# Performance work log

Hardware: AMD Instinct MI355X
Metric: run time of the kernel (lower is better)

Reference implementation:

```python
import jax, jax.numpy as jnp
import numpy as np


def _mlp(x, W1, b1, W2, b2):
    # Linear -> exact GELU (torch nn.GELU default) -> Linear
    h = jax.nn.gelu(x @ W1 + b1, approximate=False)
    return h @ W2 + b2


def setup_inputs() -> dict:
    B, L, H, NB, D, HID = 4, 4096, 16, 64, 1024, 128
    NS = H * NB
    key = jax.random.key(0)
    ks = jax.random.split(key, 6)
    theta_path = jax.random.normal(ks[0], (B, L, H, NB), dtype=jnp.float32)
    content_emb = jax.random.normal(ks[1], (B, L, D), dtype=jnp.float32)
    log_Pi = jnp.zeros((H, NB), dtype=jnp.float32)
    s1 = 1.0 / np.sqrt(D)
    s2 = 1.0 / np.sqrt(HID)
    # log_R_head: Linear(D,128) -> GELU -> Linear(128,NS), last weight scaled by 0.01, bias 0
    Wr1 = jax.random.uniform(ks[2], (D, HID), jnp.float32, -s1, s1)
    br1 = jnp.zeros((HID,), jnp.float32)
    Wr2 = jax.random.uniform(ks[3], (HID, NS), jnp.float32, -s2, s2) * 0.01
    br2 = jnp.zeros((NS,), jnp.float32)
    # measure_head: Linear(D,128) -> GELU -> Linear(128,NS)
    Wm1 = jax.random.uniform(ks[4], (D, HID), jnp.float32, -s1, s1)
    bm1 = jnp.zeros((HID,), jnp.float32)
    Wm2 = jax.random.uniform(ks[5], (HID, NS), jnp.float32, -s2, s2)
    bm2 = jnp.zeros((NS,), jnp.float32)
    return {
        "theta_path": theta_path, "content_emb": content_emb, "log_Pi": log_Pi,
        "Wr1": Wr1, "br1": br1, "Wr2": Wr2, "br2": br2,
        "Wm1": Wm1, "bm1": bm1, "Wm2": Wm2, "bm2": bm2,
    }


def reference(theta_path, content_emb, log_Pi, Wr1, br1, Wr2, br2, Wm1, bm1, Wm2, bm2):
    B, L, H, NB = theta_path.shape
    # per-token measurement noise R_t
    log_R = jnp.clip(_mlp(content_emb, Wr1, br1, Wr2, br2).reshape(B, L, H, NB), -5.0, 5.0)
    R = jnp.exp(log_R)
    # measurement z in (-pi, pi)
    z = jnp.pi * jnp.tanh(_mlp(content_emb, Wm1, bm1, Wm2, bm2).reshape(B, L, H, NB))
    diff = z - theta_path
    nu = jnp.arctan2(jnp.sin(diff), jnp.cos(diff))  # wrapped innovation
    Pi = jnp.exp(log_Pi)            # (H, NB) constant covariance
    Pi_b = Pi[None, None]           # (1,1,H,NB)
    K = Pi_b / jnp.maximum(Pi_b + R, 1e-8)  # Kalman gain
    alpha = 1.0 - K
    u = K * nu
    # scalar affine parallel scan: d[t] = alpha[t]*d[t-1] + u[t], d[-1]=0
    def combine(c1, c2):
        a1, v1 = c1
        a2, v2 = c2
        return a1 * a2, a2 * v1 + v2
    _, d = jax.lax.associative_scan(combine, (alpha, u), axis=1)
    theta_hat = theta_path + d
    return theta_hat, Pi, K, R
```

## Files before the change

kernel.cpp:

```cpp
#include <hip/hip_runtime.h>
#include <math.h>

static constexpr size_t OUT_THETA = 0;
static constexpr size_t OUT_PI    = 16777216;
static constexpr size_t OUT_K     = 16778240;
static constexpr size_t OUT_R     = 33555456;

#define PI_F     3.14159265358979323846f
#define INV2PI_F 0.15915494309189535f
#define PI2_HI   6.28318548202514648f
#define PI2_LO  -1.7484556e-7f
#define SPLIT_S  2048.0f
#define SPLIT_IS (1.0f / 2048.0f)

typedef _Float16 half8 __attribute__((ext_vector_type(8)));
typedef float    f32x4 __attribute__((ext_vector_type(4)));

__device__ __forceinline__ float gelu_f(float x) {
    return 0.5f * x * (1.0f + erff(x * 0.70710678118654752f));
}

__global__ __launch_bounds__(256) void k_prep(
    const float* __restrict__ Wr1, const float* __restrict__ Wm1,
    const float* __restrict__ Wr2, const float* __restrict__ Wm2,
    _Float16* __restrict__ W1rT, _Float16* __restrict__ W1mTh, _Float16* __restrict__ W1mTl,
    _Float16* __restrict__ W2rT, _Float16* __restrict__ W2mTh, _Float16* __restrict__ W2mTl)
{
    const int i = blockIdx.x * 256 + threadIdx.x;
    {
        const int k = i >> 7, c = i & 127;
        const int o = c * 1024 + k;
        W1rT[o] = (_Float16)Wr1[i];
        float w = Wm1[i];
        _Float16 h = (_Float16)w;
        W1mTh[o] = h;
        W1mTl[o] = (_Float16)((w - (float)h) * SPLIT_S);
    }
    {
        const int k = i >> 10, c = i & 1023;
        const int o = c * 128 + k;
        W2rT[o] = (_Float16)Wr2[i];
        float w = Wm2[i];
        _Float16 h = (_Float16)w;
        W2mTh[o] = h;
        W2mTl[o] = (_Float16)((w - (float)h) * SPLIT_S);
    }
}

__global__ __launch_bounds__(256, 3) void k_mm1(
    const float* __restrict__ X,
    const _Float16* __restrict__ WrT,
    const _Float16* __restrict__ WmTh, const _Float16* __restrict__ WmTl,
    const float* __restrict__ br1, const float* __restrict__ bm1,
    _Float16* __restrict__ OHr, _Float16* __restrict__ OHmh, _Float16* __restrict__ OHml)
{
    __shared__ _Float16 sm[15360];
    _Float16* WR = sm;
    _Float16* WH = sm + 5120;
    _Float16* WL = sm + 10240;

    const int m0   = blockIdx.x * 64;
    const int tid  = threadIdx.x;
    const int lane = tid & 63;
    const int quad = lane >> 4, l15 = lane & 15;
    const int rt   = tid >> 6;

    f32x4 accR[8] = {};
    f32x4 accA[8] = {};
    f32x4 accB[8] = {};

    const float* xp = X + (size_t)(m0 + rt * 16 + l15) * 1024 + quad * 8;
    float4 xa = *(const float4*)(xp);
    float4 xb = *(const float4*)(xp + 4);

    half8 wr[2], wh[2], wl[2];
#pragma unroll
    for (int it = 0; it < 2; ++it) {
        const int u = tid + it * 256;
        const int col = u >> 2, ws = u & 3;
        const size_t go = (size_t)col * 1024 + ws * 8;
        wr[it] = *(const half8*)(WrT  + go);
        wh[it] = *(const half8*)(WmTh + go);
        wl[it] = *(const half8*)(WmTl + go);
    }

    for (int k0 = 0; k0 < 1024; k0 += 32) {
        __syncthreads();
#pragma unroll
        for (int it = 0; it < 2; ++it) {
            const int u = tid + it * 256;
            const int col = u >> 2, ws = u & 3;
            *(half8*)&WR[col * 40 + ws * 8] = wr[it];
            *(half8*)&WH[col * 40 + ws * 8] = wh[it];
            *(half8*)&WL[col * 40 + ws * 8] = wl[it];
        }
        __syncthreads();
        half8 ah, al;
#pragma unroll
        for (int c = 0; c < 8; ++c) {
            float v = (c < 4) ? ((const float*)&xa)[c] : ((const float*)&xb)[c - 4];
            _Float16 h = (_Float16)v;
            ah[c] = h;
            al[c] = (_Float16)((v - (float)h) * SPLIT_S);
        }
        if (k0 + 32 < 1024) {
            xa = *(const float4*)(xp + k0 + 32);
            xb = *(const float4*)(xp + k0 + 36);
#pragma unroll
            for (int it = 0; it < 2; ++it) {
                const int u = tid + it * 256;
                const int col = u >> 2, ws = u & 3;
                const size_t go = (size_t)col * 1024 + k0 + 32 + ws * 8;
                wr[it] = *(const half8*)(WrT  + go);
                wh[it] = *(const half8*)(WmTh + go);
                wl[it] = *(const half8*)(WmTl + go);
            }
        }
#pragma unroll
        for (int ct = 0; ct < 8; ++ct) {
            half8 bhr = *(const half8*)&WR[(ct * 16 + l15) * 40 + quad * 8];
            accR[ct] = __builtin_amdgcn_mfma_f32_16x16x32_f16(ah, bhr, accR[ct], 0, 0, 0);
            half8 bhm = *(const half8*)&WH[(ct * 16 + l15) * 40 + quad * 8];
            accA[ct] = __builtin_amdgcn_mfma_f32_16x16x32_f16(ah, bhm, accA[ct], 0, 0, 0);
            half8 blm = *(const half8*)&WL[(ct * 16 + l15) * 40 + quad * 8];
            accB[ct] = __builtin_amdgcn_mfma_f32_16x16x32_f16(ah, blm, accB[ct], 0, 0, 0);
            accB[ct] = __builtin_amdgcn_mfma_f32_16x16x32_f16(al, bhm, accB[ct], 0, 0, 0);
        }
    }
#pragma unroll
    for (int ct = 0; ct < 8; ++ct) {
        const int col = ct * 16 + l15;
        const float bR = br1[col];
        const float bM = bm1[col];
#pragma unroll
        for (int reg = 0; reg < 4; ++reg) {
            const int token = m0 + rt * 16 + quad * 4 + reg;
            const size_t o = (size_t)token * 128 + col;
            float gr = gelu_f(accR[ct][reg] + bR);
            OHr[o] = (_Float16)gr;
            float gm = gelu_f(accA[ct][reg] + accB[ct][reg] * SPLIT_IS + bM);
            _Float16 h = (_Float16)gm;
            OHmh[o] = h;
            OHml[o] = (_Float16)((gm - (float)h) * SPLIT_S);
        }
    }
}

__global__ __launch_bounds__(256, 4) void k_mm2(
    const _Float16* __restrict__ Hr, const _Float16* __restrict__ Hmh, const _Float16* __restrict__ Hml,
    const _Float16* __restrict__ W2rT, const _Float16* __restrict__ W2mTh, const _Float16* __restrict__ W2mTl,
    const float* __restrict__ br2, const float* __restrict__ bm2,
    const float* __restrict__ log_Pi, const float* __restrict__ theta,
    float* __restrict__ out, float* __restrict__ Aws, float* __restrict__ Uws)
{
    __shared__ _Float16 sm[15360];
    _Float16* AHr = sm;
    _Float16* AHm = sm + 2560;
    _Float16* ALm = sm + 5120;
    _Float16* BHr = sm + 7680;
    _Float16* BHm = sm + 10240;
    _Float16* BLm = sm + 12800;

    const int tt = blockIdx.x;
    const int jt = blockIdx.y;
    const int m0 = tt * 64, n0 = jt * 64;
    const int tid  = threadIdx.x;
    const int lane = tid & 63;
    const int quad = lane >> 4, l15 = lane & 15;
    const int ct   = tid >> 6;
    const int row  = tid >> 2, seg = tid & 3;

    f32x4 accr[4] = {};
    f32x4 accA[4] = {};
    f32x4 accB[4] = {};

    const size_t aobase = (size_t)(m0 + row) * 128 + seg * 8;
    const size_t bobase = (size_t)(n0 + row) * 128 + seg * 8;
    half8 la = *(const half8*)(Hr    + aobase);
    half8 lb = *(const half8*)(Hmh   + aobase);
    half8 lc = *(const half8*)(Hml   + aobase);
    half8 ld = *(const half8*)(W2rT  + bobase);
    half8 le = *(const half8*)(W2mTh + bobase);
    half8 lf = *(const half8*)(W2mTl + bobase);

    for (int k0 = 0; k0 < 128; k0 += 32) {
        __syncthreads();
        const int so = row * 40 + seg * 8;
        *(half8*)&AHr[so] = la;
        *(half8*)&AHm[so] = lb;
        *(half8*)&ALm[so] = lc;
        *(half8*)&BHr[so] = ld;
        *(half8*)&BHm[so] = le;
        *(half8*)&BLm[so] = lf;
        __syncthreads();
        if (k0 + 32 < 128) {
            la = *(const half8*)(Hr    + aobase + k0 + 32);
            lb = *(const half8*)(Hmh   + aobase + k0 + 32);
            lc = *(const half8*)(Hml   + aobase + k0 + 32);
            ld = *(const half8*)(W2rT  + bobase + k0 + 32);
            le = *(const half8*)(W2mTh + bobase + k0 + 32);
            lf = *(const half8*)(W2mTl + bobase + k0 + 32);
        }
        const int bidx = (ct * 16 + l15) * 40 + quad * 8;
        half8 br_ = *(const half8*)&BHr[bidx];
        half8 bm_ = *(const half8*)&BHm[bidx];
        half8 bl_ = *(const half8*)&BLm[bidx];
#pragma unroll
        for (int rt = 0; rt < 4; ++rt) {
            const int aidx = (rt * 16 + l15) * 40 + quad * 8;
            half8 a_r = *(const half8*)&AHr[aidx];
            half8 a_h = *(const half8*)&AHm[aidx];
            half8 a_l = *(const half8*)&ALm[aidx];
            accr[rt] = __builtin_amdgcn_mfma_f32_16x16x32_f16(a_r, br_, accr[rt], 0, 0, 0);
            accA[rt] = __builtin_amdgcn_mfma_f32_16x16x32_f16(a_h, bm_, accA[rt], 0, 0, 0);
            accB[rt] = __builtin_amdgcn_mfma_f32_16x16x32_f16(a_h, bl_, accB[rt], 0, 0, 0);
            accB[rt] = __builtin_amdgcn_mfma_f32_16x16x32_f16(a_l, bm_, accB[rt], 0, 0, 0);
        }
    }

    const int col = n0 + ct * 16 + l15;
    const float Pi_  = expf(log_Pi[col]);
    const float b2rv = br2[col];
    const float b2mv = bm2[col];
    float segA[4], segU[4];
#pragma unroll
    for (int rt = 0; rt < 4; ++rt) {
        float A = 1.0f, U = 0.0f;
#pragma unroll
        for (int reg = 0; reg < 4; ++reg) {
            const int token = m0 + rt * 16 + quad * 4 + reg;
            const size_t idx = (size_t)token * 1024 + col;
            float lr = fminf(fmaxf(accr[rt][reg] + b2rv, -5.0f), 5.0f);
            float R  = expf(lr);
            float Kg = __fdividef(Pi_, fmaxf(Pi_ + R, 1e-8f));
            float zp = accA[rt][reg] + accB[rt][reg] * SPLIT_IS + b2mv;
            float z  = PI_F * tanhf(zp);
            float d  = z - theta[idx];
            float n  = rintf(d * INV2PI_F);
            float nu = fmaf(-n, PI2_HI, d);
            nu       = fmaf(-n, PI2_LO, nu);
            float u  = Kg * nu;
            float al = 1.0f - Kg;
            U = fmaf(al, U, u);
            A *= al;
            out[OUT_K + idx]     = Kg;
            out[OUT_R + idx]     = R;
            out[OUT_THETA + idx] = u;
        }
        segA[rt] = A; segU[rt] = U;
    }
    __syncthreads();
    float* cA = (float*)sm;
    float* cU = cA + 1088;
    const int colLocal = ct * 16 + l15;
#pragma unroll
    for (int rt = 0; rt < 4; ++rt) {
        cA[colLocal * 17 + rt * 4 + quad] = segA[rt];
        cU[colLocal * 17 + rt * 4 + quad] = segU[rt];
    }
    __syncthreads();
    if (tid < 64) {
        float A = 1.0f, U = 0.0f;
#pragma unroll
        for (int s = 0; s < 16; ++s) {
            float a = cA[tid * 17 + s];
            float u = cU[tid * 17 + s];
            U = fmaf(a, U, u);
            A *= a;
        }
        Aws[(size_t)tt * 1024 + n0 + tid] = A;
        Uws[(size_t)tt * 1024 + n0 + tid] = U;
    }
}

__global__ __launch_bounds__(256) void k_carry(
    const float* __restrict__ Aws, const float* __restrict__ Uws, float* __restrict__ Cws,
    const float* __restrict__ log_Pi, float* __restrict__ out)
{
    const int b  = blockIdx.x;
    const int j4 = threadIdx.x;
    if (b == 0) {
        float4 lp = *(const float4*)(log_Pi + j4 * 4);
        float4 p;
        p.x = expf(lp.x); p.y = expf(lp.y); p.z = expf(lp.z); p.w = expf(lp.w);
        *(float4*)(out + OUT_PI + j4 * 4) = p;
    }
    float4 carry = {0.0f, 0.0f, 0.0f, 0.0f};
#pragma unroll 8
    for (int c = 0; c < 64; ++c) {
        const size_t off = (size_t)(b * 64 + c) * 1024 + j4 * 4;
        float4 a = *(const float4*)(Aws + off);
        float4 u = *(const float4*)(Uws + off);
        *(float4*)(Cws + off) = carry;
        carry.x = fmaf(a.x, carry.x, u.x);
        carry.y = fmaf(a.y, carry.y, u.y);
        carry.z = fmaf(a.z, carry.z, u.z);
        carry.w = fmaf(a.w, carry.w, u.w);
    }
}

__global__ __launch_bounds__(256) void k_apply(
    const float* __restrict__ theta, const float* __restrict__ Cws, float* __restrict__ out)
{
    const int bid = blockIdx.x;
    const int c   = bid & 63;
    const int b   = bid >> 6;
    const int j0  = threadIdx.x * 4;
    float4 d = *(const float4*)(Cws + (size_t)(b * 64 + c) * 1024 + j0);
    size_t idx = (size_t)(b * 4096 + c * 64) * 1024 + j0;
    const float* __restrict__ Kbase = out + OUT_K;
#pragma unroll 4
    for (int i = 0; i < 64; ++i) {
        float4 Kg = *(const float4*)(Kbase + idx);
        float4 u  = *(const float4*)(out + idx);
        float4 th = *(const float4*)(theta + idx);
        d.x = fmaf(1.0f - Kg.x, d.x, u.x);
        d.y = fmaf(1.0f - Kg.y, d.y, u.y);
        d.z = fmaf(1.0f - Kg.z, d.z, u.z);
        d.w = fmaf(1.0f - Kg.w, d.w, u.w);
        float4 r;
        r.x = th.x + d.x; r.y = th.y + d.y; r.z = th.z + d.z; r.w = th.w + d.w;
        *(float4*)(out + idx) = r;
        idx += 1024;
    }
}

extern "C" void kernel_launch(void* const* d_in, const int* in_sizes, int n_in,
                              void* d_out, int out_size, void* d_ws, size_t ws_size,
                              hipStream_t stream)
{
    const float* theta = (const float*)d_in[0];
    const float* x     = (const float*)d_in[1];
    const float* logPi = (const float*)d_in[2];
    const float* Wr1   = (const float*)d_in[3];
    const float* br1   = (const float*)d_in[4];
    const float* Wr2   = (const float*)d_in[5];
    const float* br2   = (const float*)d_in[6];
    const float* Wm1   = (const float*)d_in[7];
    const float* bm1   = (const float*)d_in[8];
    const float* Wm2   = (const float*)d_in[9];
    const float* bm2   = (const float*)d_in[10];
    float* out = (float*)d_out;

    _Float16* Hr    = (_Float16*)d_ws;
    _Float16* Hmh   = Hr  + (size_t)16384 * 128;
    _Float16* Hml   = Hmh + (size_t)16384 * 128;
    _Float16* W1rT  = Hml + (size_t)16384 * 128;
    _Float16* W1mTh = W1rT  + 131072;
    _Float16* W1mTl = W1mTh + 131072;
    _Float16* W2rT  = W1mTl + 131072;
    _Float16* W2mTh = W2rT  + 131072;
    _Float16* W2mTl = W2mTh + 131072;
    float* Aws = (float*)(W2mTl + 131072);
    float* Uws = Aws + 262144;
    float* Cws = Uws + 262144;

    k_prep<<<512, 256, 0, stream>>>(Wr1, Wm1, Wr2, Wm2,
                                    W1rT, W1mTh, W1mTl, W2rT, W2mTh, W2mTl);
    k_mm1<<<256, 256, 0, stream>>>(x, W1rT, W1mTh, W1mTl, br1, bm1, Hr, Hmh, Hml);
    k_mm2<<<dim3(256, 16), 256, 0, stream>>>(Hr, Hmh, Hml, W2rT, W2mTh, W2mTl,
                                             br2, bm2, logPi, theta, out, Aws, Uws);
    k_carry<<<4, 256, 0, stream>>>(Aws, Uws, Cws, logPi, out);
    k_apply<<<256, 256, 0, stream>>>(theta, Cws, out);
}
```

Baseline: 470.1 us.

## Double-buffer mm1 LDS weight tiles and split scan apply into 16-row segments

k_mm1 now double-buffers the weight tiles in shared memory, so only one barrier is needed per k-step and the global loads for the next tile overlap the MFMA work. k_mm2 also emits per-16-row segment carries (A16/U16), which lets a new k_apply16 run over 1024 blocks of 16 rows each instead of 256 blocks of 64 rows, giving the final pass more parallelism. The R output uses a nontemporal store. In exchange, k_mm1 uses twice the LDS with launch bounds of 1, which lowers occupancy, and the new path needs extra workspace, falling back to the old kernel when the workspace is too small.

```diff
diff --git a/kernel.cpp b/kernel.cpp
--- a/kernel.cpp
+++ b/kernel.cpp
@@ -47,17 +47,14 @@
     }
 }
 
-__global__ __launch_bounds__(256, 3) void k_mm1(
+__global__ __launch_bounds__(256, 1) void k_mm1(
     const float* __restrict__ X,
     const _Float16* __restrict__ WrT,
     const _Float16* __restrict__ WmTh, const _Float16* __restrict__ WmTl,
     const float* __restrict__ br1, const float* __restrict__ bm1,
     _Float16* __restrict__ OHr, _Float16* __restrict__ OHmh, _Float16* __restrict__ OHml)
 {
-    __shared__ _Float16 sm[15360];
-    _Float16* WR = sm;
-    _Float16* WH = sm + 5120;
-    _Float16* WL = sm + 10240;
+    __shared__ _Float16 sm[30720];
 
     const int m0   = blockIdx.x * 64;
     const int tid  = threadIdx.x;
@@ -83,29 +80,26 @@
         wh[it] = *(const half8*)(WmTh + go);
         wl[it] = *(const half8*)(WmTl + go);
     }
+#pragma unroll
+    for (int it = 0; it < 2; ++it) {
+        const int u = tid + it * 256;
+        const int col = u >> 2, ws = u & 3;
+        *(half8*)&sm[        col * 40 + ws * 8] = wr[it];
+        *(half8*)&sm[ 5120 + col * 40 + ws * 8] = wh[it];
+        *(half8*)&sm[10240 + col * 40 + ws * 8] = wl[it];
+    }
+    __syncthreads();
 
     for (int k0 = 0; k0 < 1024; k0 += 32) {
-        __syncthreads();
-#pragma unroll
-        for (int it = 0; it < 2; ++it) {
-            const int u = tid + it * 256;
-            const int col = u >> 2, ws = u & 3;
-            *(half8*)&WR[col * 40 + ws * 8] = wr[it];
-            *(half8*)&WH[col * 40 + ws * 8] = wh[it];
-            *(half8*)&WL[col * 40 + ws * 8] = wl[it];
-        }
-        __syncthreads();
-        half8 ah, al;
-#pragma unroll
-        for (int c = 0; c < 8; ++c) {
-            float v = (c < 4) ? ((const float*)&xa)[c] : ((const float*)&xb)[c - 4];
-            _Float16 h = (_Float16)v;
-            ah[c] = h;
-            al[c] = (_Float16)((v - (float)h) * SPLIT_S);
-        }
-        if (k0 + 32 < 1024) {
-            xa = *(const float4*)(xp + k0 + 32);
-            xb = *(const float4*)(xp + k0 + 36);
+        const int cur = (k0 >> 5) & 1;
+        _Float16* WRc = sm + cur * 15360;
+        _Float16* WHc = WRc + 5120;
+        _Float16* WLc = WRc + 10240;
+        const bool hasNext = (k0 + 32 < 1024);
+        float4 nxa, nxb;
+        if (hasNext) {
+            nxa = *(const float4*)(xp + k0 + 32);
+            nxb = *(const float4*)(xp + k0 + 36);
 #pragma unroll
             for (int it = 0; it < 2; ++it) {
                 const int u = tid + it * 256;
@@ -116,16 +110,37 @@
                 wl[it] = *(const half8*)(WmTl + go);
             }
         }
+        half8 ah, al;
+#pragma unroll
+        for (int c = 0; c < 8; ++c) {
+            float v = (c < 4) ? ((const float*)&xa)[c] : ((const float*)&xb)[c - 4];
+            _Float16 h = (_Float16)v;
+            ah[c] = h;
+            al[c] = (_Float16)((v - (float)h) * SPLIT_S);
+        }
 #pragma unroll
         for (int ct = 0; ct < 8; ++ct) {
-            half8 bhr = *(const half8*)&WR[(ct * 16 + l15) * 40 + quad * 8];
+            half8 bhr = *(const half8*)&WRc[(ct * 16 + l15) * 40 + quad * 8];
             accR[ct] = __builtin_amdgcn_mfma_f32_16x16x32_f16(ah, bhr, accR[ct], 0, 0, 0);
-            half8 bhm = *(const half8*)&WH[(ct * 16 + l15) * 40 + quad * 8];
+            half8 bhm = *(const half8*)&WHc[(ct * 16 + l15) * 40 + quad * 8];
             accA[ct] = __builtin_amdgcn_mfma_f32_16x16x32_f16(ah, bhm, accA[ct], 0, 0, 0);
-            half8 blm = *(const half8*)&WL[(ct * 16 + l15) * 40 + quad * 8];
+            half8 blm = *(const half8*)&WLc[(ct * 16 + l15) * 40 + quad * 8];
             accB[ct] = __builtin_amdgcn_mfma_f32_16x16x32_f16(ah, blm, accB[ct], 0, 0, 0);
             accB[ct] = __builtin_amdgcn_mfma_f32_16x16x32_f16(al, bhm, accB[ct], 0, 0, 0);
         }
+        if (hasNext) {
+            _Float16* WRn = sm + (cur ^ 1) * 15360;
+#pragma unroll
+            for (int it = 0; it < 2; ++it) {
+                const int u = tid + it * 256;
+                const int col = u >> 2, ws = u & 3;
+                *(half8*)&WRn[        col * 40 + ws * 8] = wr[it];
+                *(half8*)&WRn[ 5120 + col * 40 + ws * 8] = wh[it];
+                *(half8*)&WRn[10240 + col * 40 + ws * 8] = wl[it];
+            }
+            xa = nxa; xb = nxb;
+        }
+        __syncthreads();
     }
 #pragma unroll
     for (int ct = 0; ct < 8; ++ct) {
@@ -151,7 +166,8 @@
     const _Float16* __restrict__ W2rT, const _Float16* __restrict__ W2mTh, const _Float16* __restrict__ W2mTl,
     const float* __restrict__ br2, const float* __restrict__ bm2,
     const float* __restrict__ log_Pi, const float* __restrict__ theta,
-    float* __restrict__ out, float* __restrict__ Aws, float* __restrict__ Uws)
+    float* __restrict__ out, float* __restrict__ Aws, float* __restrict__ Uws,
+    float* __restrict__ A16, float* __restrict__ U16)
 {
     __shared__ _Float16 sm[15360];
     _Float16* AHr = sm;
@@ -244,7 +260,7 @@
             U = fmaf(al, U, u);
             A *= al;
             out[OUT_K + idx]     = Kg;
-            out[OUT_R + idx]     = R;
+            __builtin_nontemporal_store(R, &out[OUT_R + idx]);
             out[OUT_THETA + idx] = u;
         }
         segA[rt] = A; segU[rt] = U;
@@ -262,11 +278,21 @@
     if (tid < 64) {
         float A = 1.0f, U = 0.0f;
 #pragma unroll
-        for (int s = 0; s < 16; ++s) {
-            float a = cA[tid * 17 + s];
-            float u = cU[tid * 17 + s];
-            U = fmaf(a, U, u);
-            A *= a;
+        for (int s = 0; s < 4; ++s) {
+            float A4 = 1.0f, U4 = 0.0f;
+#pragma unroll
+            for (int q = 0; q < 4; ++q) {
+                float a = cA[tid * 17 + s * 4 + q];
+                float u = cU[tid * 17 + s * 4 + q];
+                U4 = fmaf(a, U4, u);
+                A4 *= a;
+            }
+            if (A16) {
+                A16[((size_t)tt * 4 + s) * 1024 + n0 + tid] = A4;
+                U16[((size_t)tt * 4 + s) * 1024 + n0 + tid] = U4;
+            }
+            U = fmaf(A4, U, U4);
+            A *= A4;
         }
         Aws[(size_t)tt * 1024 + n0 + tid] = A;
         Uws[(size_t)tt * 1024 + n0 + tid] = U;
@@ -296,6 +322,45 @@
         carry.y = fmaf(a.y, carry.y, u.y);
         carry.z = fmaf(a.z, carry.z, u.z);
         carry.w = fmaf(a.w, carry.w, u.w);
+    }
+}
+
+__global__ __launch_bounds__(256) void k_apply16(
+    const float* __restrict__ theta, const float* __restrict__ Cws,
+    const float* __restrict__ A16, const float* __restrict__ U16,
+    float* __restrict__ out)
+{
+    const int g   = blockIdx.x;
+    const int tt  = g >> 2;
+    const int cg  = g & 3;
+    const int tid = threadIdx.x;
+    const int s   = tid >> 6;
+    const int j   = cg * 256 + (tid & 63) * 4;
+
+    float4 d = *(const float4*)(Cws + (size_t)tt * 1024 + j);
+    for (int ss = 0; ss < s; ++ss) {
+        float4 a = *(const float4*)(A16 + ((size_t)tt * 4 + ss) * 1024 + j);
+        float4 u = *(const float4*)(U16 + ((size_t)tt * 4 + ss) * 1024 + j);
+        d.x = fmaf(a.x, d.x, u.x);
+        d.y = fmaf(a.y, d.y, u.y);
+        d.z = fmaf(a.z, d.z, u.z);
+        d.w = fmaf(a.w, d.w, u.w);
+    }
+    size_t idx = (size_t)(tt * 64 + s * 16) * 1024 + j;
+    const float* __restrict__ Kbase = out + OUT_K;
+#pragma unroll 4
+    for (int i = 0; i < 16; ++i) {
+        float4 Kg = *(const float4*)(Kbase + idx);
+        float4 u  = *(const float4*)(out + idx);
+        float4 th = *(const float4*)(theta + idx);
+        d.x = fmaf(1.0f - Kg.x, d.x, u.x);
+        d.y = fmaf(1.0f - Kg.y, d.y, u.y);
+        d.z = fmaf(1.0f - Kg.z, d.z, u.z);
+        d.w = fmaf(1.0f - Kg.w, d.w, u.w);
+        float4 r;
+        r.x = th.x + d.x; r.y = th.y + d.y; r.z = th.z + d.z; r.w = th.w + d.w;
+        *(float4*)(out + idx) = r;
+        idx += 1024;
     }
 }
 
@@ -354,12 +419,22 @@
     float* Aws = (float*)(W2mTl + 131072);
     float* Uws = Aws + 262144;
     float* Cws = Uws + 262144;
+    float* A16 = Cws + 262144;
+    float* U16 = A16 + 1048576;
+    const size_t ws_need = (size_t)((char*)(U16 + 1048576) - (char*)d_ws);
+    const bool seg16 = ws_size >= ws_need;
 
     k_prep<<<512, 256, 0, stream>>>(Wr1, Wm1, Wr2, Wm2,
                                     W1rT, W1mTh, W1mTl, W2rT, W2mTh, W2mTl);
     k_mm1<<<256, 256, 0, stream>>>(x, W1rT, W1mTh, W1mTl, br1, bm1, Hr, Hmh, Hml);
     k_mm2<<<dim3(256, 16), 256, 0, stream>>>(Hr, Hmh, Hml, W2rT, W2mTh, W2mTl,
-                                             br2, bm2, logPi, theta, out, Aws, Uws);
+                                             br2, bm2, logPi, theta, out, Aws, Uws,
+                                             seg16 ? A16 : nullptr,
+                                             seg16 ? U16 : nullptr);
     k_carry<<<4, 256, 0, stream>>>(Aws, Uws, Cws, logPi, out);
-    k_apply<<<256, 256, 0, stream>>>(theta, Cws, out);
-}
+    if (seg16) {
+        k_apply16<<<1024, 256, 0, stream>>>(theta, Cws, A16, U16, out);
+    } else {
+        k_apply<<<256, 256, 0, stream>>>(theta, Cws, out);
+    }
+}
```

New measurement: 492.7 us. +4.8%, slower.

## Stage theta loads and output stores through shared memory for coalesced float4 access

Applied to the files above, without the earlier changes.

Theta tiles are first loaded into shared memory with coalesced float4 reads. The per-element R, K and u results are held in registers, then written back through the shared tile in three passes so each global store is a full-row float4. This replaces strided scalar global accesses that followed the MFMA fragment layout. The exact expf/tanhf calls are also swapped for fast __expf-based versions, which adds register pressure, extra barriers and slightly lower precision.

```diff
diff --git a/kernel.cpp b/kernel.cpp
--- a/kernel.cpp
+++ b/kernel.cpp
@@ -18,6 +18,11 @@
 
 __device__ __forceinline__ float gelu_f(float x) {
     return 0.5f * x * (1.0f + erff(x * 0.70710678118654752f));
+}
+
+__device__ __forceinline__ float tanh_fast(float x) {
+    float e = __expf(2.0f * x);
+    return 1.0f - __fdividef(2.0f, e + 1.0f);
 }
 
 __global__ __launch_bounds__(256) void k_prep(
@@ -218,24 +223,38 @@
         }
     }
 
+    float* tile = (float*)sm;
+    const int w    = tid >> 6;
+    const int trow = lane >> 4;
+    const int cf   = (lane & 15) * 4;
+
+    __syncthreads();
+#pragma unroll
+    for (int i = 0; i < 4; ++i) {
+        const int t = i * 16 + w * 4 + trow;
+        *(float4*)&tile[t * 68 + cf] =
+            *(const float4*)(theta + (size_t)(m0 + t) * 1024 + n0 + cf);
+    }
+    __syncthreads();
+
     const int col = n0 + ct * 16 + l15;
     const float Pi_  = expf(log_Pi[col]);
     const float b2rv = br2[col];
     const float b2mv = bm2[col];
+    float Rv[4][4], Kv[4][4], uv[4][4];
     float segA[4], segU[4];
 #pragma unroll
     for (int rt = 0; rt < 4; ++rt) {
         float A = 1.0f, U = 0.0f;
 #pragma unroll
         for (int reg = 0; reg < 4; ++reg) {
-            const int token = m0 + rt * 16 + quad * 4 + reg;
-            const size_t idx = (size_t)token * 1024 + col;
+            const int tl = rt * 16 + quad * 4 + reg;
             float lr = fminf(fmaxf(accr[rt][reg] + b2rv, -5.0f), 5.0f);
-            float R  = expf(lr);
+            float R  = __expf(lr);
             float Kg = __fdividef(Pi_, fmaxf(Pi_ + R, 1e-8f));
             float zp = accA[rt][reg] + accB[rt][reg] * SPLIT_IS + b2mv;
-            float z  = PI_F * tanhf(zp);
-            float d  = z - theta[idx];
+            float z  = PI_F * tanh_fast(zp);
+            float d  = z - tile[tl * 68 + ct * 16 + l15];
             float n  = rintf(d * INV2PI_F);
             float nu = fmaf(-n, PI2_HI, d);
             nu       = fmaf(-n, PI2_LO, nu);
@@ -243,12 +262,31 @@
             float al = 1.0f - Kg;
             U = fmaf(al, U, u);
             A *= al;
-            out[OUT_K + idx]     = Kg;
-            out[OUT_R + idx]     = R;
-            out[OUT_THETA + idx] = u;
+            Rv[rt][reg] = R; Kv[rt][reg] = Kg; uv[rt][reg] = u;
         }
         segA[rt] = A; segU[rt] = U;
     }
+#pragma unroll
+    for (int s = 0; s < 3; ++s) {
+        __syncthreads();
+#pragma unroll
+        for (int rt = 0; rt < 4; ++rt)
+#pragma unroll
+            for (int reg = 0; reg < 4; ++reg) {
+                const int tl = rt * 16 + quad * 4 + reg;
+                float v = (s == 0) ? uv[rt][reg] : (s == 1) ? Kv[rt][reg] : Rv[rt][reg];
+                tile[tl * 68 + ct * 16 + l15] = v;
+            }
+        __syncthreads();
+        const size_t base = (s == 0) ? OUT_THETA : (s == 1) ? OUT_K : OUT_R;
+#pragma unroll
+        for (int i = 0; i < 4; ++i) {
+            const int t = i * 16 + w * 4 + trow;
+            *(float4*)(out + base + (size_t)(m0 + t) * 1024 + n0 + cf) =
+                *(const float4*)&tile[t * 68 + cf];
+        }
+    }
+
     __syncthreads();
     float* cA = (float*)sm;
     float* cU = cA + 1088;
```

Result: faster. 435.5 us (-7.3%).
